# Kernel tuning notes

Measured on AMD Instinct MI355X. Metric: run time of the kernel, lower is better.

Reference implementation:

```python
import math
import jax, jax.numpy as jnp
import numpy as np

N, D, K = 8192, 256, 32


def setup_inputs() -> dict:
    key = jax.random.key(0)
    kx, kw, kb = jax.random.split(key, 3)
    x = jax.random.normal(kx, (N, D), dtype=jnp.float32)
    # params per _init_weights: w ~ N(1, 0.01), b ~ N(0, 0.01)
    w = 1.0 + 0.01 * jax.random.normal(kw, (K, D), dtype=jnp.float32)
    b = 0.01 * jax.random.normal(kb, (K, D), dtype=jnp.float32)
    return {"x": x, "w": w, "b": b}


def reference(x, w, b):
    # x: (N, D); w, b: (K, D)
    y1 = w[None, :, :] * (x[:, None, :] + b[None, :, :])        # (N, K, D)
    y2 = y1 * y1                                                 # (N, K, D)
    y4 = -0.5 * jnp.sum(y2, axis=-1)                             # (N, K)
    gamma = jax.nn.softmax(y4, axis=-1)                          # (N, K)
    y6 = (y2 - 1.0) * (1.0 / math.sqrt(2.0))                     # (N, K, D)
    g = gamma[:, :, None]                                        # (N, K, 1)
    n, kk, d = y1.shape
    sigma_part = (g * y6).reshape(n, kk * d)                     # (N, K*D)
    mu_part = (g * y1).reshape(n, kk * d)                        # (N, K*D)
    phi_patches = jnp.concatenate([sigma_part, mu_part], axis=-1)
    return jnp.mean(phi_patches, axis=0)                         # (2*K*D,)
```

## Files before the change

kernel.cpp:

```cpp
#include <hip/hip_runtime.h>
#include <math.h>

#define Nn 8192
#define Dd 256
#define Kk 32

#define P_OFF   0
#define P2_OFF  4194304
#define SP_OFF  4325376
#define SP2_OFF 4333568

__global__ __launch_bounds__(512, 4) void fused_kernel(const float* __restrict__ x,
                                                       const float* __restrict__ w,
                                                       const float* __restrict__ b,
                                                       float* __restrict__ ws) {
    __shared__ __align__(16) float uS[8192];
    __shared__ __align__(16) float vS[8192];
    __shared__ __align__(16) float gS[1024];

    float* P  = ws + P_OFF;
    float* Sp = ws + SP_OFF;
    int tid = threadIdx.x;
    int blk = blockIdx.x;

    {
        const float4* w4 = (const float4*)w;
        const float4* b4 = (const float4*)b;
        float4* uD = (float4*)uS;
        float4* vD = (float4*)vS;
        #pragma unroll
        for (int i = 0; i < 4; ++i) {
            int e4 = tid + i * 512;
            int k  = e4 >> 6;
            int d4 = e4 & 63;
            float4 wv = w4[e4];
            float4 bv = b4[e4];
            float4 vv = {wv.x * bv.x, wv.y * bv.y, wv.z * bv.z, wv.w * bv.w};
            uD[d4 * 32 + k] = wv;
            vD[d4 * 32 + k] = vv;
        }
    }
    __syncthreads();

    {
        int lane = tid & 63;
        int wave = tid >> 6;
        int k = lane & 31;
        int h = lane >> 5;
        int r0 = wave * 4;
        size_t rowbase = (size_t)blk * 32 + r0;

        const float4* uS4 = (const float4*)uS;
        const float4* vS4 = (const float4*)vS;
        const float4* xr0 = (const float4*)(x + (rowbase + 0) * Dd);
        const float4* xr1 = (const float4*)(x + (rowbase + 1) * Dd);
        const float4* xr2 = (const float4*)(x + (rowbase + 2) * Dd);
        const float4* xr3 = (const float4*)(x + (rowbase + 3) * Dd);

        float4 a0 = {0.f,0.f,0.f,0.f}, a1 = a0, a2 = a0, a3 = a0;

        #pragma unroll 4
        for (int i = 0; i < 32; ++i) {
            int ii = h * 32 + i;
            float4 u  = uS4[ii * 32 + k];
            float4 v  = vS4[ii * 32 + k];
            float4 x0 = xr0[ii];
            float4 x1 = xr1[ii];
            float4 x2 = xr2[ii];
            float4 x3 = xr3[ii];
            float y;
            y = fmaf(u.x, x0.x, v.x); a0.x = fmaf(y, y, a0.x);
            y = fmaf(u.y, x0.y, v.y); a0.y = fmaf(y, y, a0.y);
            y = fmaf(u.z, x0.z, v.z); a0.z = fmaf(y, y, a0.z);
            y = fmaf(u.w, x0.w, v.w); a0.w = fmaf(y, y, a0.w);
            y = fmaf(u.x, x1.x, v.x); a1.x = fmaf(y, y, a1.x);
            y = fmaf(u.y, x1.y, v.y); a1.y = fmaf(y, y, a1.y);
            y = fmaf(u.z, x1.z, v.z); a1.z = fmaf(y, y, a1.z);
            y = fmaf(u.w, x1.w, v.w); a1.w = fmaf(y, y, a1.w);
            y = fmaf(u.x, x2.x, v.x); a2.x = fmaf(y, y, a2.x);
            y = fmaf(u.y, x2.y, v.y); a2.y = fmaf(y, y, a2.y);
            y = fmaf(u.z, x2.z, v.z); a2.z = fmaf(y, y, a2.z);
            y = fmaf(u.w, x2.w, v.w); a2.w = fmaf(y, y, a2.w);
            y = fmaf(u.x, x3.x, v.x); a3.x = fmaf(y, y, a3.x);
            y = fmaf(u.y, x3.y, v.y); a3.y = fmaf(y, y, a3.y);
            y = fmaf(u.z, x3.z, v.z); a3.z = fmaf(y, y, a3.z);
            y = fmaf(u.w, x3.w, v.w); a3.w = fmaf(y, y, a3.w);
        }

        float s0 = (a0.x + a0.y) + (a0.z + a0.w);
        float s1 = (a1.x + a1.y) + (a1.z + a1.w);
        float s2 = (a2.x + a2.y) + (a2.z + a2.w);
        float s3 = (a3.x + a3.y) + (a3.z + a3.w);
        s0 += __shfl_xor(s0, 32);
        s1 += __shfl_xor(s1, 32);
        s2 += __shfl_xor(s2, 32);
        s3 += __shfl_xor(s3, 32);
        float y40 = -0.5f * s0, y41 = -0.5f * s1, y42 = -0.5f * s2, y43 = -0.5f * s3;

        float m0 = y40, m1 = y41, m2 = y42, m3 = y43;
        #pragma unroll
        for (int o = 16; o >= 1; o >>= 1) {
            m0 = fmaxf(m0, __shfl_xor(m0, o));
            m1 = fmaxf(m1, __shfl_xor(m1, o));
            m2 = fmaxf(m2, __shfl_xor(m2, o));
            m3 = fmaxf(m3, __shfl_xor(m3, o));
        }
        float e0 = __expf(y40 - m0), e1 = __expf(y41 - m1);
        float e2 = __expf(y42 - m2), e3 = __expf(y43 - m3);
        float t0 = e0, t1 = e1, t2 = e2, t3 = e3;
        #pragma unroll
        for (int o = 16; o >= 1; o >>= 1) {
            t0 += __shfl_xor(t0, o);
            t1 += __shfl_xor(t1, o);
            t2 += __shfl_xor(t2, o);
            t3 += __shfl_xor(t3, o);
        }
        if (h == 0) {
            gS[(r0 + 0) * 32 + k] = e0 / t0;
            gS[(r0 + 1) * 32 + k] = e1 / t1;
            gS[(r0 + 2) * 32 + k] = e2 / t2;
            gS[(r0 + 3) * 32 + k] = e3 / t3;
        }
    }
    __syncthreads();

    if (tid < 32) {
        float s0 = 0.f, s1 = 0.f, s2 = 0.f, s3 = 0.f;
        #pragma unroll
        for (int r = 0; r < 32; r += 4) {
            s0 += gS[(r + 0) * 32 + tid];
            s1 += gS[(r + 1) * 32 + tid];
            s2 += gS[(r + 2) * 32 + tid];
            s3 += gS[(r + 3) * 32 + tid];
        }
        Sp[blk * 32 + tid] = (s0 + s1) + (s2 + s3);
    }

    {
        int kh = tid >> 8;
        int d  = tid & 255;
        const float* xcol = x + ((size_t)blk * 32) * Dd + d;
        const float4* gS4 = (const float4*)gS;

        float aG[16], aH[16];
        #pragma unroll
        for (int j = 0; j < 16; ++j) { aG[j] = 0.f; aH[j] = 0.f; }

        #pragma unroll 4
        for (int r = 0; r < 32; ++r) {
            float xv = xcol[(size_t)r * Dd];
            float xx = xv * xv;
            #pragma unroll
            for (int q = 0; q < 4; ++q) {
                float4 gv = gS4[r * 8 + kh * 4 + q];
                aG[4*q+0] = fmaf(gv.x, xv, aG[4*q+0]); aH[4*q+0] = fmaf(gv.x, xx, aH[4*q+0]);
                aG[4*q+1] = fmaf(gv.y, xv, aG[4*q+1]); aH[4*q+1] = fmaf(gv.y, xx, aH[4*q+1]);
                aG[4*q+2] = fmaf(gv.z, xv, aG[4*q+2]); aH[4*q+2] = fmaf(gv.z, xx, aH[4*q+2]);
                aG[4*q+3] = fmaf(gv.w, xv, aG[4*q+3]); aH[4*q+3] = fmaf(gv.w, xx, aH[4*q+3]);
            }
        }

        #pragma unroll
        for (int j = 0; j < 16; ++j) {
            int k = kh * 16 + j;
            P[((size_t)(k * 2 + 0) * 256 + blk) * 256 + d] = aG[j];
            P[((size_t)(k * 2 + 1) * 256 + blk) * 256 + d] = aH[j];
        }
    }
}

__global__ __launch_bounds__(256) void red1_kernel(float* __restrict__ ws) {
    const float* P  = ws + P_OFF;
    const float* Sp = ws + SP_OFF;
    float* P2  = ws + P2_OFF;
    float* Sp2 = ws + SP2_OFF;
    int tid = threadIdx.x;
    int k  = blockIdx.x >> 4;
    int gh = (blockIdx.x >> 3) & 1;
    int c  = blockIdx.x & 7;

    const float* p = P + ((size_t)(k * 2 + gh) * 256 + c * 32) * 256 + tid;
    float s0 = 0.f, s1 = 0.f, s2 = 0.f, s3 = 0.f;
    #pragma unroll
    for (int i = 0; i < 32; i += 4) {
        s0 += p[(size_t)(i + 0) * 256];
        s1 += p[(size_t)(i + 1) * 256];
        s2 += p[(size_t)(i + 2) * 256];
        s3 += p[(size_t)(i + 3) * 256];
    }
    P2[((size_t)(k * 2 + gh) * 8 + c) * 256 + tid] = (s0 + s1) + (s2 + s3);

    if (gh == 0 && tid == 0) {
        float t0 = 0.f, t1 = 0.f, t2 = 0.f, t3 = 0.f;
        #pragma unroll
        for (int i = 0; i < 32; i += 4) {
            t0 += Sp[(c * 32 + i + 0) * 32 + k];
            t1 += Sp[(c * 32 + i + 1) * 32 + k];
            t2 += Sp[(c * 32 + i + 2) * 32 + k];
            t3 += Sp[(c * 32 + i + 3) * 32 + k];
        }
        Sp2[k * 8 + c] = (t0 + t1) + (t2 + t3);
    }
}

__global__ __launch_bounds__(256) void red2_kernel(const float* __restrict__ w,
                                                   const float* __restrict__ b,
                                                   const float* __restrict__ ws,
                                                   float* __restrict__ out) {
    const float* P2  = ws + P2_OFF;
    const float* Sp2 = ws + SP2_OFF;
    int k = blockIdx.x, d = threadIdx.x;

    const float* pg = P2 + (size_t)(k * 2 + 0) * 8 * 256 + d;
    const float* ph = P2 + (size_t)(k * 2 + 1) * 8 * 256 + d;
    float Gv = 0.f, Hv = 0.f, sv = 0.f;
    #pragma unroll
    for (int c = 0; c < 8; ++c) {
        Gv += pg[c * 256];
        Hv += ph[c * 256];
        sv += Sp2[k * 8 + c];
    }

    int idx = k * Dd + d;
    float wv = w[idx], bv = b[idx];
    const float invN = 1.0f / 8192.0f;
    const float c2 = 0.70710678118654752440f * invN;
    float mu = wv * (Gv + bv * sv) * invN;
    float w2 = wv * wv;
    float sg = (w2 * (Hv + 2.0f * bv * Gv + bv * bv * sv) - sv) * c2;
    out[idx] = sg;
    out[Kk * Dd + idx] = mu;
}

extern "C" void kernel_launch(void* const* d_in, const int* in_sizes, int n_in,
                              void* d_out, int out_size, void* d_ws, size_t ws_size,
                              hipStream_t stream) {
    const float* x = (const float*)d_in[0];
    const float* w = (const float*)d_in[1];
    const float* b = (const float*)d_in[2];
    float* out = (float*)d_out;
    float* ws = (float*)d_ws;

    hipLaunchKernelGGL(fused_kernel, dim3(256), dim3(512), 0, stream, x, w, b, ws);
    hipLaunchKernelGGL(red1_kernel,  dim3(512), dim3(256), 0, stream, ws);
    hipLaunchKernelGGL(red2_kernel,  dim3(32),  dim3(256), 0, stream, w, b, ws, out);
}
```

Before: 85.70 us.

## Double block threads, pad LDS weight tables, move Sp reduction into final kernel

The fused kernel now runs 1024 threads per block. Each wave handles 2 rows in the distance phase and 8 mixture components per thread in the accumulation phase, which halves per-thread register arrays and raises the number of waves per block. The u/v weight tables in shared memory get a stride of 33 float4s to reduce bank conflicts. The column sum of softmax weights moves from red1 into red2, which now does a shuffle-based reduction. The costs are a larger block with fewer resident blocks per CU, and x rows are re-read by more threads.

```diff
diff --git a/kernel.cpp b/kernel.cpp
--- a/kernel.cpp
+++ b/kernel.cpp
@@ -8,15 +8,14 @@
 #define P_OFF   0
 #define P2_OFF  4194304
 #define SP_OFF  4325376
-#define SP2_OFF 4333568
-
-__global__ __launch_bounds__(512, 4) void fused_kernel(const float* __restrict__ x,
-                                                       const float* __restrict__ w,
-                                                       const float* __restrict__ b,
-                                                       float* __restrict__ ws) {
-    __shared__ __align__(16) float uS[8192];
-    __shared__ __align__(16) float vS[8192];
-    __shared__ __align__(16) float gS[1024];
+
+__global__ __launch_bounds__(1024) void fused_kernel(const float* __restrict__ x,
+                                                     const float* __restrict__ w,
+                                                     const float* __restrict__ b,
+                                                     float* __restrict__ ws) {
+    __shared__ __align__(16) float4 uS4[64 * 33];
+    __shared__ __align__(16) float4 vS4[64 * 33];
+    __shared__ __align__(16) float  gS[1024];
 
     float* P  = ws + P_OFF;
     float* Sp = ws + SP_OFF;
@@ -26,18 +25,16 @@
     {
         const float4* w4 = (const float4*)w;
         const float4* b4 = (const float4*)b;
-        float4* uD = (float4*)uS;
-        float4* vD = (float4*)vS;
-        #pragma unroll
-        for (int i = 0; i < 4; ++i) {
-            int e4 = tid + i * 512;
+        #pragma unroll
+        for (int i = 0; i < 2; ++i) {
+            int e4 = tid + i * 1024;
             int k  = e4 >> 6;
             int d4 = e4 & 63;
             float4 wv = w4[e4];
             float4 bv = b4[e4];
             float4 vv = {wv.x * bv.x, wv.y * bv.y, wv.z * bv.z, wv.w * bv.w};
-            uD[d4 * 32 + k] = wv;
-            vD[d4 * 32 + k] = vv;
+            uS4[d4 * 33 + k] = wv;
+            vS4[d4 * 33 + k] = vv;
         }
     }
     __syncthreads();
@@ -47,27 +44,21 @@
         int wave = tid >> 6;
         int k = lane & 31;
         int h = lane >> 5;
-        int r0 = wave * 4;
+        int r0 = wave * 2;
         size_t rowbase = (size_t)blk * 32 + r0;
 
-        const float4* uS4 = (const float4*)uS;
-        const float4* vS4 = (const float4*)vS;
         const float4* xr0 = (const float4*)(x + (rowbase + 0) * Dd);
         const float4* xr1 = (const float4*)(x + (rowbase + 1) * Dd);
-        const float4* xr2 = (const float4*)(x + (rowbase + 2) * Dd);
-        const float4* xr3 = (const float4*)(x + (rowbase + 3) * Dd);
-
-        float4 a0 = {0.f,0.f,0.f,0.f}, a1 = a0, a2 = a0, a3 = a0;
-
-        #pragma unroll 4
+
+        float4 a0 = {0.f, 0.f, 0.f, 0.f}, a1 = a0;
+
+        #pragma unroll 8
         for (int i = 0; i < 32; ++i) {
             int ii = h * 32 + i;
-            float4 u  = uS4[ii * 32 + k];
-            float4 v  = vS4[ii * 32 + k];
+            float4 u  = uS4[ii * 33 + k];
+            float4 v  = vS4[ii * 33 + k];
             float4 x0 = xr0[ii];
             float4 x1 = xr1[ii];
-            float4 x2 = xr2[ii];
-            float4 x3 = xr3[ii];
             float y;
             y = fmaf(u.x, x0.x, v.x); a0.x = fmaf(y, y, a0.x);
             y = fmaf(u.y, x0.y, v.y); a0.y = fmaf(y, y, a0.y);
@@ -77,49 +68,30 @@
             y = fmaf(u.y, x1.y, v.y); a1.y = fmaf(y, y, a1.y);
             y = fmaf(u.z, x1.z, v.z); a1.z = fmaf(y, y, a1.z);
             y = fmaf(u.w, x1.w, v.w); a1.w = fmaf(y, y, a1.w);
-            y = fmaf(u.x, x2.x, v.x); a2.x = fmaf(y, y, a2.x);
-            y = fmaf(u.y, x2.y, v.y); a2.y = fmaf(y, y, a2.y);
-            y = fmaf(u.z, x2.z, v.z); a2.z = fmaf(y, y, a2.z);
-            y = fmaf(u.w, x2.w, v.w); a2.w = fmaf(y, y, a2.w);
-            y = fmaf(u.x, x3.x, v.x); a3.x = fmaf(y, y, a3.x);
-            y = fmaf(u.y, x3.y, v.y); a3.y = fmaf(y, y, a3.y);
-            y = fmaf(u.z, x3.z, v.z); a3.z = fmaf(y, y, a3.z);
-            y = fmaf(u.w, x3.w, v.w); a3.w = fmaf(y, y, a3.w);
         }
 
         float s0 = (a0.x + a0.y) + (a0.z + a0.w);
         float s1 = (a1.x + a1.y) + (a1.z + a1.w);
-        float s2 = (a2.x + a2.y) + (a2.z + a2.w);
-        float s3 = (a3.x + a3.y) + (a3.z + a3.w);
         s0 += __shfl_xor(s0, 32);
         s1 += __shfl_xor(s1, 32);
-        s2 += __shfl_xor(s2, 32);
-        s3 += __shfl_xor(s3, 32);
-        float y40 = -0.5f * s0, y41 = -0.5f * s1, y42 = -0.5f * s2, y43 = -0.5f * s3;
-
-        float m0 = y40, m1 = y41, m2 = y42, m3 = y43;
+        float y40 = -0.5f * s0, y41 = -0.5f * s1;
+
+        float m0 = y40, m1 = y41;
         #pragma unroll
         for (int o = 16; o >= 1; o >>= 1) {
             m0 = fmaxf(m0, __shfl_xor(m0, o));
             m1 = fmaxf(m1, __shfl_xor(m1, o));
-            m2 = fmaxf(m2, __shfl_xor(m2, o));
-            m3 = fmaxf(m3, __shfl_xor(m3, o));
         }
         float e0 = __expf(y40 - m0), e1 = __expf(y41 - m1);
-        float e2 = __expf(y42 - m2), e3 = __expf(y43 - m3);
-        float t0 = e0, t1 = e1, t2 = e2, t3 = e3;
+        float t0 = e0, t1 = e1;
         #pragma unroll
         for (int o = 16; o >= 1; o >>= 1) {
             t0 += __shfl_xor(t0, o);
             t1 += __shfl_xor(t1, o);
-            t2 += __shfl_xor(t2, o);
-            t3 += __shfl_xor(t3, o);
         }
         if (h == 0) {
             gS[(r0 + 0) * 32 + k] = e0 / t0;
             gS[(r0 + 1) * 32 + k] = e1 / t1;
-            gS[(r0 + 2) * 32 + k] = e2 / t2;
-            gS[(r0 + 3) * 32 + k] = e3 / t3;
         }
     }
     __syncthreads();
@@ -137,22 +109,22 @@
     }
 
     {
-        int kh = tid >> 8;
+        int kq = tid >> 8;
         int d  = tid & 255;
         const float* xcol = x + ((size_t)blk * 32) * Dd + d;
         const float4* gS4 = (const float4*)gS;
 
-        float aG[16], aH[16];
-        #pragma unroll
-        for (int j = 0; j < 16; ++j) { aG[j] = 0.f; aH[j] = 0.f; }
+        float aG[8], aH[8];
+        #pragma unroll
+        for (int j = 0; j < 8; ++j) { aG[j] = 0.f; aH[j] = 0.f; }
 
         #pragma unroll 4
         for (int r = 0; r < 32; ++r) {
             float xv = xcol[(size_t)r * Dd];
             float xx = xv * xv;
             #pragma unroll
-            for (int q = 0; q < 4; ++q) {
-                float4 gv = gS4[r * 8 + kh * 4 + q];
+            for (int q = 0; q < 2; ++q) {
+                float4 gv = gS4[r * 8 + kq * 2 + q];
                 aG[4*q+0] = fmaf(gv.x, xv, aG[4*q+0]); aH[4*q+0] = fmaf(gv.x, xx, aH[4*q+0]);
                 aG[4*q+1] = fmaf(gv.y, xv, aG[4*q+1]); aH[4*q+1] = fmaf(gv.y, xx, aH[4*q+1]);
                 aG[4*q+2] = fmaf(gv.z, xv, aG[4*q+2]); aH[4*q+2] = fmaf(gv.z, xx, aH[4*q+2]);
@@ -161,8 +133,8 @@
         }
 
         #pragma unroll
-        for (int j = 0; j < 16; ++j) {
-            int k = kh * 16 + j;
+        for (int j = 0; j < 8; ++j) {
+            int k = kq * 8 + j;
             P[((size_t)(k * 2 + 0) * 256 + blk) * 256 + d] = aG[j];
             P[((size_t)(k * 2 + 1) * 256 + blk) * 256 + d] = aH[j];
         }
@@ -170,10 +142,8 @@
 }
 
 __global__ __launch_bounds__(256) void red1_kernel(float* __restrict__ ws) {
-    const float* P  = ws + P_OFF;
-    const float* Sp = ws + SP_OFF;
-    float* P2  = ws + P2_OFF;
-    float* Sp2 = ws + SP2_OFF;
+    const float* P = ws + P_OFF;
+    float* P2 = ws + P2_OFF;
     int tid = threadIdx.x;
     int k  = blockIdx.x >> 4;
     int gh = (blockIdx.x >> 3) & 1;
@@ -189,36 +159,31 @@
         s3 += p[(size_t)(i + 3) * 256];
     }
     P2[((size_t)(k * 2 + gh) * 8 + c) * 256 + tid] = (s0 + s1) + (s2 + s3);
-
-    if (gh == 0 && tid == 0) {
-        float t0 = 0.f, t1 = 0.f, t2 = 0.f, t3 = 0.f;
-        #pragma unroll
-        for (int i = 0; i < 32; i += 4) {
-            t0 += Sp[(c * 32 + i + 0) * 32 + k];
-            t1 += Sp[(c * 32 + i + 1) * 32 + k];
-            t2 += Sp[(c * 32 + i + 2) * 32 + k];
-            t3 += Sp[(c * 32 + i + 3) * 32 + k];
-        }
-        Sp2[k * 8 + c] = (t0 + t1) + (t2 + t3);
-    }
 }
 
 __global__ __launch_bounds__(256) void red2_kernel(const float* __restrict__ w,
                                                    const float* __restrict__ b,
                                                    const float* __restrict__ ws,
                                                    float* __restrict__ out) {
-    const float* P2  = ws + P2_OFF;
-    const float* Sp2 = ws + SP2_OFF;
+    const float* P2 = ws + P2_OFF;
+    const float* Sp = ws + SP_OFF;
+    __shared__ float sred[4];
     int k = blockIdx.x, d = threadIdx.x;
+
+    float sv_part = Sp[d * 32 + k];
+    #pragma unroll
+    for (int o = 32; o >= 1; o >>= 1) sv_part += __shfl_xor(sv_part, o);
+    if ((d & 63) == 0) sred[d >> 6] = sv_part;
+    __syncthreads();
+    float sv = (sred[0] + sred[1]) + (sred[2] + sred[3]);
 
     const float* pg = P2 + (size_t)(k * 2 + 0) * 8 * 256 + d;
     const float* ph = P2 + (size_t)(k * 2 + 1) * 8 * 256 + d;
-    float Gv = 0.f, Hv = 0.f, sv = 0.f;
+    float Gv = 0.f, Hv = 0.f;
     #pragma unroll
     for (int c = 0; c < 8; ++c) {
         Gv += pg[c * 256];
         Hv += ph[c * 256];
-        sv += Sp2[k * 8 + c];
     }
 
     int idx = k * Dd + d;
@@ -241,7 +206,7 @@
     float* out = (float*)d_out;
     float* ws = (float*)d_ws;
 
-    hipLaunchKernelGGL(fused_kernel, dim3(256), dim3(512), 0, stream, x, w, b, ws);
-    hipLaunchKernelGGL(red1_kernel,  dim3(512), dim3(256), 0, stream, ws);
-    hipLaunchKernelGGL(red2_kernel,  dim3(32),  dim3(256), 0, stream, w, b, ws, out);
-}
+    hipLaunchKernelGGL(fused_kernel, dim3(256), dim3(1024), 0, stream, x, w, b, ws);
+    hipLaunchKernelGGL(red1_kernel,  dim3(512), dim3(256),  0, stream, ws);
+    hipLaunchKernelGGL(red2_kernel,  dim3(32),  dim3(256),  0, stream, w, b, ws, out);
+}
```

After: 83.92 us. 2.1% less time.

## Merge two reduction kernels into one and pad shared-memory u/v tables

Applied to the files above, without the earlier changes.

Replaces the two-stage reduction (red1 over 512 blocks writing partials, then red2) with a single 32-block, 1024-thread kernel that sums all 256 block partials per k and applies the final epilogue. This removes one launch and the intermediate P2/Sp2 round trip. The u/v shared tables are padded to a stride of 33 float4 to reduce LDS bank conflicts, and the occupancy hint on the fused kernel is dropped. The cost is that the reduction now runs on only 32 blocks, each reading a long strided column, which leaves most of the GPU idle during that phase.

```diff
diff --git a/kernel.cpp b/kernel.cpp
--- a/kernel.cpp
+++ b/kernel.cpp
@@ -6,17 +6,15 @@
 #define Kk 32
 
 #define P_OFF   0
-#define P2_OFF  4194304
-#define SP_OFF  4325376
-#define SP2_OFF 4333568
-
-__global__ __launch_bounds__(512, 4) void fused_kernel(const float* __restrict__ x,
-                                                       const float* __restrict__ w,
-                                                       const float* __restrict__ b,
-                                                       float* __restrict__ ws) {
-    __shared__ __align__(16) float uS[8192];
-    __shared__ __align__(16) float vS[8192];
-    __shared__ __align__(16) float gS[1024];
+#define SP_OFF  4194304
+
+__global__ __launch_bounds__(512) void fused_kernel(const float* __restrict__ x,
+                                                    const float* __restrict__ w,
+                                                    const float* __restrict__ b,
+                                                    float* __restrict__ ws) {
+    __shared__ __align__(16) float4 uS4[64 * 33];
+    __shared__ __align__(16) float4 vS4[64 * 33];
+    __shared__ __align__(16) float  gS[1024];
 
     float* P  = ws + P_OFF;
     float* Sp = ws + SP_OFF;
@@ -26,8 +24,6 @@
     {
         const float4* w4 = (const float4*)w;
         const float4* b4 = (const float4*)b;
-        float4* uD = (float4*)uS;
-        float4* vD = (float4*)vS;
         #pragma unroll
         for (int i = 0; i < 4; ++i) {
             int e4 = tid + i * 512;
@@ -36,8 +32,8 @@
             float4 wv = w4[e4];
             float4 bv = b4[e4];
             float4 vv = {wv.x * bv.x, wv.y * bv.y, wv.z * bv.z, wv.w * bv.w};
-            uD[d4 * 32 + k] = wv;
-            vD[d4 * 32 + k] = vv;
+            uS4[d4 * 33 + k] = wv;
+            vS4[d4 * 33 + k] = vv;
         }
     }
     __syncthreads();
@@ -50,8 +46,6 @@
         int r0 = wave * 4;
         size_t rowbase = (size_t)blk * 32 + r0;
 
-        const float4* uS4 = (const float4*)uS;
-        const float4* vS4 = (const float4*)vS;
         const float4* xr0 = (const float4*)(x + (rowbase + 0) * Dd);
         const float4* xr1 = (const float4*)(x + (rowbase + 1) * Dd);
         const float4* xr2 = (const float4*)(x + (rowbase + 2) * Dd);
@@ -62,8 +56,8 @@
         #pragma unroll 4
         for (int i = 0; i < 32; ++i) {
             int ii = h * 32 + i;
-            float4 u  = uS4[ii * 32 + k];
-            float4 v  = vS4[ii * 32 + k];
+            float4 u  = uS4[ii * 33 + k];
+            float4 v  = vS4[ii * 33 + k];
             float4 x0 = xr0[ii];
             float4 x1 = xr1[ii];
             float4 x2 = xr2[ii];
@@ -169,67 +163,52 @@
     }
 }
 
-__global__ __launch_bounds__(256) void red1_kernel(float* __restrict__ ws) {
+__global__ __launch_bounds__(1024) void red_kernel(const float* __restrict__ w,
+                                                   const float* __restrict__ b,
+                                                   const float* __restrict__ ws,
+                                                   float* __restrict__ out) {
     const float* P  = ws + P_OFF;
     const float* Sp = ws + SP_OFF;
-    float* P2  = ws + P2_OFF;
-    float* Sp2 = ws + SP2_OFF;
-    int tid = threadIdx.x;
-    int k  = blockIdx.x >> 4;
-    int gh = (blockIdx.x >> 3) & 1;
-    int c  = blockIdx.x & 7;
-
-    const float* p = P + ((size_t)(k * 2 + gh) * 256 + c * 32) * 256 + tid;
+    __shared__ float acc[4][256];
+    __shared__ float sred[16];
+    int t = threadIdx.x;
+    int k = blockIdx.x;
+    int gh = t >> 9;
+    int bh = (t >> 8) & 1;
+    int d  = t & 255;
+
+    const float* p = P + ((size_t)(k * 2 + gh) * 256 + bh * 128) * 256 + d;
     float s0 = 0.f, s1 = 0.f, s2 = 0.f, s3 = 0.f;
-    #pragma unroll
-    for (int i = 0; i < 32; i += 4) {
+    #pragma unroll 8
+    for (int i = 0; i < 128; i += 4) {
         s0 += p[(size_t)(i + 0) * 256];
         s1 += p[(size_t)(i + 1) * 256];
         s2 += p[(size_t)(i + 2) * 256];
         s3 += p[(size_t)(i + 3) * 256];
     }
-    P2[((size_t)(k * 2 + gh) * 8 + c) * 256 + tid] = (s0 + s1) + (s2 + s3);
-
-    if (gh == 0 && tid == 0) {
-        float t0 = 0.f, t1 = 0.f, t2 = 0.f, t3 = 0.f;
-        #pragma unroll
-        for (int i = 0; i < 32; i += 4) {
-            t0 += Sp[(c * 32 + i + 0) * 32 + k];
-            t1 += Sp[(c * 32 + i + 1) * 32 + k];
-            t2 += Sp[(c * 32 + i + 2) * 32 + k];
-            t3 += Sp[(c * 32 + i + 3) * 32 + k];
-        }
-        Sp2[k * 8 + c] = (t0 + t1) + (t2 + t3);
-    }
-}
-
-__global__ __launch_bounds__(256) void red2_kernel(const float* __restrict__ w,
-                                                   const float* __restrict__ b,
-                                                   const float* __restrict__ ws,
-                                                   float* __restrict__ out) {
-    const float* P2  = ws + P2_OFF;
-    const float* Sp2 = ws + SP2_OFF;
-    int k = blockIdx.x, d = threadIdx.x;
-
-    const float* pg = P2 + (size_t)(k * 2 + 0) * 8 * 256 + d;
-    const float* ph = P2 + (size_t)(k * 2 + 1) * 8 * 256 + d;
-    float Gv = 0.f, Hv = 0.f, sv = 0.f;
+    acc[gh * 2 + bh][d] = (s0 + s1) + (s2 + s3);
+
+    float sv_part = 0.f;
+    if (t < 256) sv_part = Sp[t * 32 + k];
     #pragma unroll
-    for (int c = 0; c < 8; ++c) {
-        Gv += pg[c * 256];
-        Hv += ph[c * 256];
-        sv += Sp2[k * 8 + c];
-    }
-
-    int idx = k * Dd + d;
-    float wv = w[idx], bv = b[idx];
-    const float invN = 1.0f / 8192.0f;
-    const float c2 = 0.70710678118654752440f * invN;
-    float mu = wv * (Gv + bv * sv) * invN;
-    float w2 = wv * wv;
-    float sg = (w2 * (Hv + 2.0f * bv * Gv + bv * bv * sv) - sv) * c2;
-    out[idx] = sg;
-    out[Kk * Dd + idx] = mu;
+    for (int o = 32; o >= 1; o >>= 1) sv_part += __shfl_xor(sv_part, o);
+    if ((t & 63) == 0) sred[t >> 6] = sv_part;
+    __syncthreads();
+
+    if (t < 256) {
+        float sv = (sred[0] + sred[1]) + (sred[2] + sred[3]);
+        float Gv = acc[0][d] + acc[1][d];
+        float Hv = acc[2][d] + acc[3][d];
+        int idx = k * Dd + d;
+        float wv = w[idx], bv = b[idx];
+        const float invN = 1.0f / 8192.0f;
+        const float c2 = 0.70710678118654752440f * invN;
+        float mu = wv * (Gv + bv * sv) * invN;
+        float w2 = wv * wv;
+        float sg = (w2 * (Hv + 2.0f * bv * Gv + bv * bv * sv) - sv) * c2;
+        out[idx] = sg;
+        out[Kk * Dd + idx] = mu;
+    }
 }
 
 extern "C" void kernel_launch(void* const* d_in, const int* in_sizes, int n_in,
@@ -241,7 +220,6 @@
     float* out = (float*)d_out;
     float* ws = (float*)d_ws;
 
-    hipLaunchKernelGGL(fused_kernel, dim3(256), dim3(512), 0, stream, x, w, b, ws);
-    hipLaunchKernelGGL(red1_kernel,  dim3(512), dim3(256), 0, stream, ws);
-    hipLaunchKernelGGL(red2_kernel,  dim3(32),  dim3(256), 0, stream, w, b, ws, out);
+    hipLaunchKernelGGL(fused_kernel, dim3(256), dim3(512),  0, stream, x, w, b, ws);
+    hipLaunchKernelGGL(red_kernel,   dim3(32),  dim3(1024), 0, stream, w, b, ws, out);
 }
```

New measurement: 87.34 us. About the same (+1.9%).
